# Kernel tuning notes

Hardware: AMD Instinct MI355X
Metric: run time of the kernel (lower is better)

The kernel has to match this reference:

```python
import jax, jax.numpy as jnp
import numpy as np

N_NODES = 50000
N_EDGES = 10000
NNZ = 1600000
IN_DIM = 256
OUT_DIM = 128


def setup_inputs() -> dict:
    key = jax.random.key(0)
    k1, k2, k3, k4, k5 = jax.random.split(key, 5)
    X = jax.random.normal(k1, (N_NODES, IN_DIM), dtype=jnp.float32)
    theta = jax.random.normal(k2, (IN_DIM, OUT_DIM), dtype=jnp.float32) * (1.0 / np.sqrt(IN_DIM))
    bias = jax.random.normal(k3, (OUT_DIM,), dtype=jnp.float32) * 0.01
    node_idx = jax.random.randint(k4, (NNZ,), 0, N_NODES, dtype=jnp.int32)
    hyedge_idx = jax.random.randint(k5, (NNZ,), 0, N_EDGES, dtype=jnp.int32)
    return {
        "X": X,
        "theta": theta,
        "bias": bias,
        "node_idx": node_idx,
        "hyedge_idx": hyedge_idx,
        "num_nodes": N_NODES,
        "num_edges": N_EDGES,
    }


def reference(X, theta, bias, node_idx, hyedge_idx, num_nodes, num_edges):
    # Dense transform: [N, in] @ [in, out] -> [N, out]
    Xt = X @ theta
    # MA_v: vertex -> hyperedge aggregation (gather by node_idx, scatter_add by hyedge_idx)
    Y = jax.ops.segment_sum(Xt[node_idx], hyedge_idx, num_segments=num_edges)  # [M, out]
    # MA_e: hyperedge -> vertex aggregation (gather by hyedge_idx, scatter_add by node_idx)
    X_new = jax.ops.segment_sum(Y[hyedge_idx], node_idx, num_segments=num_nodes)  # [N, out]
    # U_v: bias add
    return X_new + bias
```

## Files before the change

### kernel.cpp

```cpp
#include <hip/hip_runtime.h>
#include <hip/hip_bf16.h>

#define NN 50000
#define NE 10000
#define KD 256
#define MD 128

#define NCAP 76

#define RNG 4
#define RDIV 12500
#define ERCAP 96

#define NB_E 313
#define NB_N 196
#define NBT  (NB_E + NB_N)
#define CCAP_E 5760
#define CCAP_N 8960

#define GEMM_BLKS ((NN + 255) / 256)
#define NCB 256
#define CPB 6272
#define RPT ((CPB + 511) / 512)

#define AGG_BLKS ((NE + 7) / 8 * RNG)

typedef __attribute__((ext_vector_type(8))) short short8;
typedef __attribute__((ext_vector_type(4))) float f32x4;

union ABfrag { short8 s; unsigned u[4]; };

__device__ inline unsigned pack_bf2(float a, float b) {
    __hip_bfloat162 h = __float22bfloat162_rn(make_float2(a, b));
    return *reinterpret_cast<unsigned*>(&h);
}

__device__ inline unsigned short bf16_1(float a) {
    __hip_bfloat16 h = __float2bfloat16(a);
    return *reinterpret_cast<unsigned short*>(&h);
}

__device__ inline float bf_lo(unsigned v) { return __uint_as_float(v << 16); }
__device__ inline float bf_hi(unsigned v) { return __uint_as_float(v & 0xffff0000u); }

__device__ inline void exscan_block(const int* __restrict__ cnt, int* __restrict__ lst,
                                    int n, int* buf, int tid) {
    int v = (tid < n) ? cnt[tid] : 0;
    buf[tid] = v;
    __syncthreads();
    #pragma unroll
    for (int s = 1; s < 512; s <<= 1) {
        int t = (tid >= s) ? buf[tid - s] : 0;
        __syncthreads();
        buf[tid] += t;
        __syncthreads();
    }
    if (tid < n) lst[tid] = buf[tid] - v;
    __syncthreads();
}

__global__ __launch_bounds__(256) void prep_theta(const float* __restrict__ Th,
                                                  unsigned short* __restrict__ tT,
                                                  int* __restrict__ ccur) {
    int tid = threadIdx.x;
    if (blockIdx.x == 0) { ccur[tid] = 0; ccur[tid + 256] = 0; }
    int gid = blockIdx.x * 256 + tid;
    int k = gid >> 7, c = gid & 127;
    tT[(size_t)c * KD + k] = bf16_1(Th[(size_t)k * MD + c]);
}

__global__ __launch_bounds__(512) void gemm_coarse(const float* __restrict__ X,
                                                   const unsigned short* __restrict__ tT,
                                                   unsigned short* __restrict__ XtU, int N,
                                                   const int* __restrict__ nidx,
                                                   const int* __restrict__ eidx,
                                                   int* __restrict__ ccur,
                                                   unsigned* __restrict__ coarse_e,
                                                   unsigned* __restrict__ coarse_n, int nnz) {
    __shared__ unsigned srt[CPB];
    __shared__ int cntE[NB_E], lstE[NB_E], gbE[NB_E];
    __shared__ int cntN[NB_N], lstN[NB_N], gbN[NB_N];
    const int tid = threadIdx.x;

    if (blockIdx.x >= NCB) {
        const int w  = tid >> 6;
        const int l  = tid & 63;
        const int lr = l & 15;
        const int lk = l >> 4;
        const int row0 = (blockIdx.x - NCB) * 256 + w * 32;
        const int rowA = row0 + lr;
        const int rowB = row0 + 16 + lr;

        f32x4 acc0[8], acc1[8];
        #pragma unroll
        for (int ct = 0; ct < 8; ++ct) {
            acc0[ct] = (f32x4){0.f, 0.f, 0.f, 0.f};
            acc1[ct] = (f32x4){0.f, 0.f, 0.f, 0.f};
        }

        const short8* tTv = (const short8*)tT;
        #pragma unroll
        for (int ks = 0; ks < 8; ++ks) {
            ABfrag a0, a1;
            if (rowA < N) {
                const float* xp = X + (size_t)rowA * KD + ks * 32 + lk * 8;
                float4 v0 = *(const float4*)(xp);
                float4 v1 = *(const float4*)(xp + 4);
                a0.u[0] = pack_bf2(v0.x, v0.y);
                a0.u[1] = pack_bf2(v0.z, v0.w);
                a0.u[2] = pack_bf2(v1.x, v1.y);
                a0.u[3] = pack_bf2(v1.z, v1.w);
            } else a0.u[0] = a0.u[1] = a0.u[2] = a0.u[3] = 0u;
            if (rowB < N) {
                const float* xp = X + (size_t)rowB * KD + ks * 32 + lk * 8;
                float4 v0 = *(const float4*)(xp);
                float4 v1 = *(const float4*)(xp + 4);
                a1.u[0] = pack_bf2(v0.x, v0.y);
                a1.u[1] = pack_bf2(v0.z, v0.w);
                a1.u[2] = pack_bf2(v1.x, v1.y);
                a1.u[3] = pack_bf2(v1.z, v1.w);
            } else a1.u[0] = a1.u[1] = a1.u[2] = a1.u[3] = 0u;

            #pragma unroll
            for (int ct = 0; ct < 8; ++ct) {
                ABfrag b;
                b.s = tTv[(size_t)(ct * 16 + lr) * 32 + ks * 4 + lk];
                acc0[ct] = __builtin_amdgcn_mfma_f32_16x16x32_bf16(a0.s, b.s, acc0[ct], 0, 0, 0);
                acc1[ct] = __builtin_amdgcn_mfma_f32_16x16x32_bf16(a1.s, b.s, acc1[ct], 0, 0, 0);
            }
        }

        #pragma unroll
        for (int ct = 0; ct < 8; ++ct) {
            #pragma unroll
            for (int i = 0; i < 4; ++i) {
                int rA = row0 + lk * 4 + i;
                int rB = row0 + 16 + lk * 4 + i;
                if (rA < N) XtU[(size_t)rA * MD + ct * 16 + lr] = bf16_1(acc0[ct][i]);
                if (rB < N) XtU[(size_t)rB * MD + ct * 16 + lr] = bf16_1(acc1[ct][i]);
            }
        }
        return;
    }

    const int cbid = blockIdx.x;
    int C  = (nnz + NCB - 1) / NCB;
    if (C > CPB) C = CPB;
    const int k0 = cbid * C;
    int k1 = k0 + C; if (k1 > nnz) k1 = nnz;
    const int nk = k1 - k0;

    for (int j = tid; j < NB_E; j += 512) cntE[j] = 0;
    for (int j = tid; j < NB_N; j += 512) cntN[j] = 0;
    __syncthreads();

    unsigned rr[RPT];
    #pragma unroll
    for (int it = 0; it < RPT; ++it) {
        int i = tid + it * 512;
        unsigned r = 0u;
        if (i < nk) {
            int e = eidx[k0 + i], n = nidx[k0 + i];
            r = ((unsigned)n << 14) | (unsigned)e;
            atomicAdd(&cntE[e >> 5], 1);
            atomicAdd(&cntN[n >> 8], 1);
        }
        rr[it] = r;
    }
    __syncthreads();

    exscan_block(cntE, lstE, NB_E, (int*)srt, tid);
    exscan_block(cntN, lstN, NB_N, (int*)srt, tid);
    for (int j = tid; j < NB_E; j += 512) {
        int c = cntE[j];
        gbE[j] = c ? atomicAdd(&ccur[j], c) : 0;
    }
    for (int j = tid; j < NB_N; j += 512) {
        int c = cntN[j];
        gbN[j] = c ? atomicAdd(&ccur[NB_E + j], c) : 0;
    }
    __syncthreads();
    for (int j = tid; j < NB_E; j += 512) cntE[j] = 0;
    for (int j = tid; j < NB_N; j += 512) cntN[j] = 0;
    __syncthreads();

    #pragma unroll
    for (int it = 0; it < RPT; ++it) {
        int i = tid + it * 512;
        if (i < nk) {
            unsigned r = rr[it];
            int b = (r & 0x3FFF) >> 5;
            int rk = atomicAdd(&cntE[b], 1);
            srt[lstE[b] + rk] = r;
        }
    }
    __syncthreads();
    for (int p = tid; p < nk; p += 512) {
        unsigned r = srt[p];
        int b = (r & 0x3FFF) >> 5;
        int g = gbE[b] + (p - lstE[b]);
        if (g < CCAP_E) coarse_e[(size_t)b * CCAP_E + g] = r;
    }
    __syncthreads();

    #pragma unroll
    for (int it = 0; it < RPT; ++it) {
        int i = tid + it * 512;
        if (i < nk) {
            unsigned r = rr[it];
            int b = (int)(r >> 14) >> 8;
            int rk = atomicAdd(&cntN[b], 1);
            srt[lstN[b] + rk] = r;
        }
    }
    __syncthreads();
    for (int p = tid; p < nk; p += 512) {
        unsigned r = srt[p];
        int b = (int)(r >> 14) >> 8;
        int g = gbN[b] + (p - lstN[b]);
        if (g < CCAP_N) coarse_n[(size_t)b * CCAP_N + g] = r;
    }
}

__global__ __launch_bounds__(512) void fine_e(const unsigned* __restrict__ coarse_e,
                                              const int* __restrict__ ccur,
                                              unsigned short* __restrict__ e_slots,
                                              int* __restrict__ e_cnt) {
    __shared__ unsigned srt[CCAP_E];
    __shared__ int cnt[128], lst[128];
    const int tid = threadIdx.x;
    const int b = blockIdx.x;

    const unsigned* buf = coarse_e + (size_t)b * CCAP_E;
    int m = ccur[b]; if (m > CCAP_E) m = CCAP_E;

    for (int j = tid; j < 128; j += 512) cnt[j] = 0;
    __syncthreads();
    for (int i = tid; i < m; i += 512) {
        unsigned r = buf[i];
        int e = r & 0x3FFF;
        int n = (int)(r >> 14);
        atomicAdd(&cnt[((e & 31) << 2) | (n / RDIV)], 1);
    }
    __syncthreads();
    exscan_block(cnt, lst, 128, (int*)srt, tid);
    if (tid < 128) {
        int e = b * 32 + (tid >> 2);
        if (e < NE) {
            int c = cnt[tid]; if (c > ERCAP) c = ERCAP;
            e_cnt[e * RNG + (tid & 3)] = c;
        }
    }
    __syncthreads();
    for (int j = tid; j < 128; j += 512) cnt[j] = 0;
    __syncthreads();
    for (int i = tid; i < m; i += 512) {
        unsigned r = buf[i];
        int e = r & 0x3FFF;
        unsigned n = r >> 14;
        int li = ((e & 31) << 2) | ((int)n / RDIV);
        int rk = atomicAdd(&cnt[li], 1);
        srt[lst[li] + rk] = ((unsigned)li << 16) | n;
    }
    __syncthreads();
    for (int p = tid; p < m; p += 512) {
        unsigned v = srt[p];
        int li = (int)(v >> 16);
        int lr = p - lst[li];
        if (lr < ERCAP) {
            int e = b * 32 + (li >> 2);
            e_slots[((size_t)e * RNG + (li & 3)) * ERCAP + lr] = (unsigned short)(v & 0xFFFF);
        }
    }
}

__global__ __launch_bounds__(512) void fine_n_agg_ve(const unsigned* __restrict__ coarse_n,
                                                     const int* __restrict__ ccur,
                                                     unsigned short* __restrict__ n_slots,
                                                     int* __restrict__ n_cnt,
                                                     const unsigned* __restrict__ XtB,
                                                     const int* __restrict__ e_cnt,
                                                     const unsigned short* __restrict__ e_slots,
                                                     unsigned* __restrict__ P) {
    __shared__ unsigned srt[CCAP_N];
    __shared__ int cnt[256], lst[256];
    const int tid = threadIdx.x;

    if (blockIdx.x < NB_N) {
        const int bb = blockIdx.x;
        const unsigned* buf = coarse_n + (size_t)bb * CCAP_N;
        int m = ccur[NB_E + bb]; if (m > CCAP_N) m = CCAP_N;

        for (int j = tid; j < 256; j += 512) cnt[j] = 0;
        __syncthreads();
        for (int i = tid; i < m; i += 512) {
            unsigned r = buf[i];
            atomicAdd(&cnt[(r >> 14) & 255], 1);
        }
        __syncthreads();
        exscan_block(cnt, lst, 256, (int*)srt, tid);
        if (tid < 256) {
            int g = bb * 256 + tid;
            if (g < NN) {
                int c = cnt[tid]; if (c > NCAP) c = NCAP;
                n_cnt[g] = c;
            }
        }
        __syncthreads();
        for (int j = tid; j < 256; j += 512) cnt[j] = 0;
        __syncthreads();
        for (int i = tid; i < m; i += 512) {
            unsigned r = buf[i];
            int k = (r >> 14) & 255;
            int rk = atomicAdd(&cnt[k], 1);
            srt[lst[k] + rk] = ((unsigned)k << 16) | (r & 0x3FFF);
        }
        __syncthreads();
        for (int p = tid; p < m; p += 512) {
            unsigned v = srt[p];
            int k = (int)(v >> 16);
            int lr = p - lst[k];
            if (lr < NCAP) {
                int g = bb * 256 + k;
                n_slots[(size_t)g * NCAP + lr] = (unsigned short)(v & 0x3FFF);
            }
        }
        return;
    }

    const int wid = blockIdx.x - NB_N;
    const int r = wid & 3;
    const int g = wid >> 2;
    int wave = g * 8 + (tid >> 6);
    int l    = tid & 63;
    const int grp = l >> 3, sub = l & 7;
    int ec = e_cnt[wave * RNG + r]; if (ec > ERCAP) ec = ERCAP;
    const unsigned short* slots = e_slots + ((size_t)wave * RNG + r) * ERCAP;
    const uint4* Xv = (const uint4*)XtB;

    float a[16];
    #pragma unroll
    for (int i = 0; i < 16; ++i) a[i] = 0.f;

    for (int c = 0; c < ec; c += 64) {
        int m = ec - c; if (m > 64) m = 64;
        int idx = (c + l < ec) ? (int)slots[c + l] : 0;
        for (int j = 0; j < m; j += 8) {
            int mem = j + grp;
            bool valid = mem < m;
            int n = __shfl(idx, valid ? mem : 0);
            const uint4* row = Xv + (size_t)n * 16 + sub * 2;
            uint4 v0 = row[0];
            uint4 v1 = row[1];
            if (valid) {
                a[0]  += bf_lo(v0.x); a[1]  += bf_hi(v0.x);
                a[2]  += bf_lo(v0.y); a[3]  += bf_hi(v0.y);
                a[4]  += bf_lo(v0.z); a[5]  += bf_hi(v0.z);
                a[6]  += bf_lo(v0.w); a[7]  += bf_hi(v0.w);
                a[8]  += bf_lo(v1.x); a[9]  += bf_hi(v1.x);
                a[10] += bf_lo(v1.y); a[11] += bf_hi(v1.y);
                a[12] += bf_lo(v1.z); a[13] += bf_hi(v1.z);
                a[14] += bf_lo(v1.w); a[15] += bf_hi(v1.w);
            }
        }
    }
    #pragma unroll
    for (int i = 0; i < 16; ++i) {
        a[i] += __shfl_xor(a[i], 8);
        a[i] += __shfl_xor(a[i], 16);
        a[i] += __shfl_xor(a[i], 32);
    }
    if (l < 8) {
        uint4 o0 = make_uint4(pack_bf2(a[0],  a[1]),  pack_bf2(a[2],  a[3]),
                              pack_bf2(a[4],  a[5]),  pack_bf2(a[6],  a[7]));
        uint4 o1 = make_uint4(pack_bf2(a[8],  a[9]),  pack_bf2(a[10], a[11]),
                              pack_bf2(a[12], a[13]), pack_bf2(a[14], a[15]));
        uint4* prow = (uint4*)P + ((size_t)r * NE + wave) * 16 + sub * 2;
        prow[0] = o0;
        prow[1] = o1;
    }
}

__global__ __launch_bounds__(256) void reduce_y(const unsigned* __restrict__ P,
                                                unsigned* __restrict__ YB) {
    int gid = blockIdx.x * 256 + threadIdx.x;
    if (gid >= NE * 64) return;
    float a = 0.f, b = 0.f;
    #pragma unroll
    for (int r = 0; r < RNG; ++r) {
        unsigned v = P[(size_t)r * NE * 64 + gid];
        a += bf_lo(v);
        b += bf_hi(v);
    }
    YB[gid] = pack_bf2(a, b);
}

__global__ __launch_bounds__(256) void agg_ev(const unsigned* __restrict__ YB,
                                              const int* __restrict__ n_cnt,
                                              const unsigned short* __restrict__ n_slots,
                                              const float* __restrict__ bias,
                                              float* __restrict__ out) {
    int wave = blockIdx.x * 4 + (threadIdx.x >> 6);
    int l    = threadIdx.x & 63;
    if (wave >= NN) return;
    const int grp = l >> 3, sub = l & 7;
    int cnt = n_cnt[wave]; if (cnt > NCAP) cnt = NCAP;
    const unsigned short* slots = n_slots + (size_t)wave * NCAP;
    const uint4* Yv = (const uint4*)YB;

    float a[16];
    #pragma unroll
    for (int i = 0; i < 16; ++i) a[i] = 0.f;

    for (int c = 0; c < cnt; c += 64) {
        int m = cnt - c; if (m > 64) m = 64;
        int idx = (c + l < cnt) ? (int)slots[c + l] : 0;
        for (int j = 0; j < m; j += 8) {
            int mem = j + grp;
            bool valid = mem < m;
            int e = __shfl(idx, valid ? mem : 0);
            const uint4* row = Yv + (size_t)e * 16 + sub * 2;
            uint4 v0 = row[0];
            uint4 v1 = row[1];
            if (valid) {
                a[0]  += bf_lo(v0.x); a[1]  += bf_hi(v0.x);
                a[2]  += bf_lo(v0.y); a[3]  += bf_hi(v0.y);
                a[4]  += bf_lo(v0.z); a[5]  += bf_hi(v0.z);
                a[6]  += bf_lo(v0.w); a[7]  += bf_hi(v0.w);
                a[8]  += bf_lo(v1.x); a[9]  += bf_hi(v1.x);
                a[10] += bf_lo(v1.y); a[11] += bf_hi(v1.y);
                a[12] += bf_lo(v1.z); a[13] += bf_hi(v1.z);
                a[14] += bf_lo(v1.w); a[15] += bf_hi(v1.w);
            }
        }
    }
    #pragma unroll
    for (int i = 0; i < 16; ++i) {
        a[i] += __shfl_xor(a[i], 8);
        a[i] += __shfl_xor(a[i], 16);
        a[i] += __shfl_xor(a[i], 32);
    }
    if (l < 8) {
        float4* orow = (float4*)(out + (size_t)wave * MD);
        #pragma unroll
        for (int q = 0; q < 4; ++q) {
            float4 bq = ((const float4*)bias)[sub * 4 + q];
            float4 o = make_float4(a[q * 4 + 0] + bq.x, a[q * 4 + 1] + bq.y,
                                   a[q * 4 + 2] + bq.z, a[q * 4 + 3] + bq.w);
            orow[sub * 4 + q] = o;
        }
    }
}

extern "C" void kernel_launch(void* const* d_in, const int* in_sizes, int n_in,
                              void* d_out, int out_size, void* d_ws, size_t ws_size,
                              hipStream_t stream) {
    const float* X     = (const float*)d_in[0];
    const float* theta = (const float*)d_in[1];
    const float* bias  = (const float*)d_in[2];
    const int*   nidx  = (const int*)d_in[3];
    const int*   eidx  = (const int*)d_in[4];
    float*       out   = (float*)d_out;

    const int N   = in_sizes[0] / KD;
    const int nnz = in_sizes[3];

    char* w = (char*)d_ws;
    unsigned*       XtB      = (unsigned*)w;       w += (size_t)NN * MD * 2;
    unsigned*       YB       = (unsigned*)w;       w += (size_t)NE * MD * 2;
    int*            e_cnt    = (int*)w;            w += (size_t)NE * RNG * 4;
    int*            n_cnt    = (int*)w;            w += (size_t)NN * 4;
    int*            ccur     = (int*)w;            w += (size_t)512 * 4;
    unsigned short* thetaT   = (unsigned short*)w; w += (size_t)MD * KD * 2;
    unsigned*       P        = (unsigned*)w;       w += (size_t)RNG * NE * 64 * 4;
    unsigned*       coarse_e = (unsigned*)w;       w += (size_t)NB_E * CCAP_E * 4;
    unsigned*       coarse_n = (unsigned*)w;       w += (size_t)NB_N * CCAP_N * 4;
    unsigned short* e_slots  = (unsigned short*)w; w += (size_t)NE * RNG * ERCAP * 2;
    unsigned short* n_slots  = (unsigned short*)w;

    prep_theta<<<(MD * KD) / 256, 256, 0, stream>>>(theta, thetaT, ccur);

    gemm_coarse<<<NCB + GEMM_BLKS, 512, 0, stream>>>(X, thetaT, (unsigned short*)XtB, N,
                                                     nidx, eidx, ccur,
                                                     coarse_e, coarse_n, nnz);

    fine_e<<<NB_E, 512, 0, stream>>>(coarse_e, ccur, e_slots, e_cnt);

    fine_n_agg_ve<<<NB_N + AGG_BLKS, 512, 0, stream>>>(coarse_n, ccur, n_slots, n_cnt,
                                                       XtB, e_cnt, e_slots, P);

    reduce_y<<<(NE * 64 + 255) / 256, 256, 0, stream>>>(P, YB);

    agg_ev<<<(NN + 3) / 4, 256, 0, stream>>>(YB, n_cnt, n_slots, bias, out);
}
```

Measured before the change: 126.3 us.

## Run coarse binning and GEMM tile serially in each block with a shuffle scan

Each of the 256 coarse-binning blocks now also computes one GEMM row tile after finishing its binning work, instead of launching separate GEMM blocks alongside them. The grid shrinks from coarse+GEMM blocks to only NCB blocks. The two separate LDS exclusive scans over edge and node bins are merged into one wave-shuffle scan over all bins, with node bin offsets shifted by nk. This removes scan barriers and extra blocks. The cost is that work which could run in parallel on separate blocks now runs back to back inside a block, which lengthens the critical path per block.

```diff
diff --git a/kernel.cpp b/kernel.cpp
--- a/kernel.cpp
+++ b/kernel.cpp
@@ -18,8 +18,8 @@
 #define CCAP_E 5760
 #define CCAP_N 8960
 
-#define GEMM_BLKS ((NN + 255) / 256)
 #define NCB 256
+#define GEMM_TILES ((NN + 255) / 256)
 #define CPB 6272
 #define RPT ((CPB + 511) / 512)
 
@@ -69,7 +69,7 @@
     tT[(size_t)c * KD + k] = bf16_1(Th[(size_t)k * MD + c]);
 }
 
-__global__ __launch_bounds__(512) void gemm_coarse(const float* __restrict__ X,
+__global__ __launch_bounds__(512) void coarse_gemm(const float* __restrict__ X,
                                                    const unsigned short* __restrict__ tT,
                                                    unsigned short* __restrict__ XtU, int N,
                                                    const int* __restrict__ nidx,
@@ -78,16 +78,110 @@
                                                    unsigned* __restrict__ coarse_e,
                                                    unsigned* __restrict__ coarse_n, int nnz) {
     __shared__ unsigned srt[CPB];
-    __shared__ int cntE[NB_E], lstE[NB_E], gbE[NB_E];
-    __shared__ int cntN[NB_N], lstN[NB_N], gbN[NB_N];
+    __shared__ int cnt[NBT], lst[NBT], gb[NBT];
+    __shared__ int wsum[8], wpre[8];
     const int tid = threadIdx.x;
-
-    if (blockIdx.x >= NCB) {
-        const int w  = tid >> 6;
-        const int l  = tid & 63;
-        const int lr = l & 15;
-        const int lk = l >> 4;
-        const int row0 = (blockIdx.x - NCB) * 256 + w * 32;
+    const int wv = tid >> 6, lane = tid & 63;
+
+    {
+        const int cbid = blockIdx.x;
+        int C = (nnz + NCB - 1) / NCB;
+        if (C > CPB) C = CPB;
+        const int k0 = cbid * C;
+        int k1 = k0 + C; if (k1 > nnz) k1 = nnz;
+        const int nk = k1 - k0;
+
+        for (int j = tid; j < NBT; j += 512) cnt[j] = 0;
+        __syncthreads();
+
+        unsigned rr[RPT];
+        #pragma unroll
+        for (int it = 0; it < RPT; ++it) {
+            int i = tid + it * 512;
+            unsigned r = 0u;
+            if (i < nk) {
+                int e = eidx[k0 + i], n = nidx[k0 + i];
+                r = ((unsigned)n << 14) | (unsigned)e;
+                atomicAdd(&cnt[e >> 5], 1);
+                atomicAdd(&cnt[NB_E + (n >> 8)], 1);
+            }
+            rr[it] = r;
+        }
+        __syncthreads();
+
+        {
+            int myv = (tid < NBT) ? cnt[tid] : 0;
+            int v = myv;
+            #pragma unroll
+            for (int s = 1; s < 64; s <<= 1) {
+                int t = __shfl_up(v, s);
+                if (lane >= s) v += t;
+            }
+            if (lane == 63) wsum[wv] = v;
+            __syncthreads();
+            if (wv == 0) {
+                int u = (lane < 8) ? wsum[lane] : 0;
+                #pragma unroll
+                for (int s = 1; s < 8; s <<= 1) {
+                    int t = __shfl_up(u, s);
+                    if (lane >= s) u += t;
+                }
+                if (lane < 8) wpre[lane] = u - wsum[lane];
+            }
+            __syncthreads();
+            if (tid < NBT) lst[tid] = v - myv + wpre[wv];
+            __syncthreads();
+        }
+
+        for (int j = tid; j < NBT; j += 512) {
+            int c = cnt[j];
+            gb[j] = c ? atomicAdd(&ccur[j], c) : 0;
+            cnt[j] = 0;
+        }
+        __syncthreads();
+
+        #pragma unroll
+        for (int it = 0; it < RPT; ++it) {
+            int i = tid + it * 512;
+            if (i < nk) {
+                unsigned r = rr[it];
+                int b = (r & 0x3FFF) >> 5;
+                int rk = atomicAdd(&cnt[b], 1);
+                srt[lst[b] + rk] = r;
+            }
+        }
+        __syncthreads();
+        for (int p = tid; p < nk; p += 512) {
+            unsigned r = srt[p];
+            int b = (r & 0x3FFF) >> 5;
+            int g = gb[b] + (p - lst[b]);
+            if (g < CCAP_E) coarse_e[(size_t)b * CCAP_E + g] = r;
+        }
+        __syncthreads();
+
+        #pragma unroll
+        for (int it = 0; it < RPT; ++it) {
+            int i = tid + it * 512;
+            if (i < nk) {
+                unsigned r = rr[it];
+                int b = NB_E + ((int)(r >> 14) >> 8);
+                int rk = atomicAdd(&cnt[b], 1);
+                srt[(lst[b] - nk) + rk] = r;
+            }
+        }
+        __syncthreads();
+        for (int p = tid; p < nk; p += 512) {
+            unsigned r = srt[p];
+            int b = NB_E + ((int)(r >> 14) >> 8);
+            int g = gb[b] + (p - (lst[b] - nk));
+            if (g < CCAP_N) coarse_n[(size_t)(b - NB_E) * CCAP_N + g] = r;
+        }
+    }
+
+    if (blockIdx.x < GEMM_TILES) {
+        const int lr = lane & 15;
+        const int lk = lane >> 4;
+        const int row0 = blockIdx.x * 256 + wv * 32;
         const int rowA = row0 + lr;
         const int rowB = row0 + 16 + lr;
 
@@ -140,85 +234,6 @@
                 if (rB < N) XtU[(size_t)rB * MD + ct * 16 + lr] = bf16_1(acc1[ct][i]);
             }
         }
-        return;
-    }
-
-    const int cbid = blockIdx.x;
-    int C  = (nnz + NCB - 1) / NCB;
-    if (C > CPB) C = CPB;
-    const int k0 = cbid * C;
-    int k1 = k0 + C; if (k1 > nnz) k1 = nnz;
-    const int nk = k1 - k0;
-
-    for (int j = tid; j < NB_E; j += 512) cntE[j] = 0;
-    for (int j = tid; j < NB_N; j += 512) cntN[j] = 0;
-    __syncthreads();
-
-    unsigned rr[RPT];
-    #pragma unroll
-    for (int it = 0; it < RPT; ++it) {
-        int i = tid + it * 512;
-        unsigned r = 0u;
-        if (i < nk) {
-            int e = eidx[k0 + i], n = nidx[k0 + i];
-            r = ((unsigned)n << 14) | (unsigned)e;
-            atomicAdd(&cntE[e >> 5], 1);
-            atomicAdd(&cntN[n >> 8], 1);
-        }
-        rr[it] = r;
-    }
-    __syncthreads();
-
-    exscan_block(cntE, lstE, NB_E, (int*)srt, tid);
-    exscan_block(cntN, lstN, NB_N, (int*)srt, tid);
-    for (int j = tid; j < NB_E; j += 512) {
-        int c = cntE[j];
-        gbE[j] = c ? atomicAdd(&ccur[j], c) : 0;
-    }
-    for (int j = tid; j < NB_N; j += 512) {
-        int c = cntN[j];
-        gbN[j] = c ? atomicAdd(&ccur[NB_E + j], c) : 0;
-    }
-    __syncthreads();
-    for (int j = tid; j < NB_E; j += 512) cntE[j] = 0;
-    for (int j = tid; j < NB_N; j += 512) cntN[j] = 0;
-    __syncthreads();
-
-    #pragma unroll
-    for (int it = 0; it < RPT; ++it) {
-        int i = tid + it * 512;
-        if (i < nk) {
-            unsigned r = rr[it];
-            int b = (r & 0x3FFF) >> 5;
-            int rk = atomicAdd(&cntE[b], 1);
-            srt[lstE[b] + rk] = r;
-        }
-    }
-    __syncthreads();
-    for (int p = tid; p < nk; p += 512) {
-        unsigned r = srt[p];
-        int b = (r & 0x3FFF) >> 5;
-        int g = gbE[b] + (p - lstE[b]);
-        if (g < CCAP_E) coarse_e[(size_t)b * CCAP_E + g] = r;
-    }
-    __syncthreads();
-
-    #pragma unroll
-    for (int it = 0; it < RPT; ++it) {
-        int i = tid + it * 512;
-        if (i < nk) {
-            unsigned r = rr[it];
-            int b = (int)(r >> 14) >> 8;
-            int rk = atomicAdd(&cntN[b], 1);
-            srt[lstN[b] + rk] = r;
-        }
-    }
-    __syncthreads();
-    for (int p = tid; p < nk; p += 512) {
-        unsigned r = srt[p];
-        int b = (int)(r >> 14) >> 8;
-        int g = gbN[b] + (p - lstN[b]);
-        if (g < CCAP_N) coarse_n[(size_t)b * CCAP_N + g] = r;
     }
 }
 
@@ -480,9 +495,9 @@
 
     prep_theta<<<(MD * KD) / 256, 256, 0, stream>>>(theta, thetaT, ccur);
 
-    gemm_coarse<<<NCB + GEMM_BLKS, 512, 0, stream>>>(X, thetaT, (unsigned short*)XtB, N,
-                                                     nidx, eidx, ccur,
-                                                     coarse_e, coarse_n, nnz);
+    coarse_gemm<<<NCB, 512, 0, stream>>>(X, thetaT, (unsigned short*)XtB, N,
+                                         nidx, eidx, ccur,
+                                         coarse_e, coarse_n, nnz);
 
     fine_e<<<NB_E, 512, 0, stream>>>(coarse_e, ccur, e_slots, e_cnt);
 
```

Result: slower. 133.3 us (+5.6%).
